# Performance work log

Measured on AMD Instinct MI355X. Metric: run time of the kernel, lower is better.

## Reference

```python
import jax, jax.numpy as jnp
import numpy as np

B, T, INP_DIM, H = 32, 2000, 4, 512
TC = 0.01  # t_const


def setup_inputs() -> dict:
    key = jax.random.key(0)
    ks = jax.random.split(key, 10)
    inp = jax.random.normal(ks[0], (B, T, INP_DIM), dtype=jnp.float32)
    hn = jax.random.uniform(ks[1], (1, B, 2 * H), dtype=jnp.float32)
    x = jnp.zeros((1, B, 2 * H), jnp.float32)
    inhib_stim = jnp.zeros((B, T, 2 * H), jnp.float32)
    u = lambda k, s, hi: jax.random.uniform(k, s, jnp.float32, 0.0, hi)
    str2str_w = u(ks[2], (H, H), 0.01)
    alm2alm_w = u(ks[3], (H, H), 0.01)
    alm2str_w = u(ks[4], (H, H), 0.01)
    str2alm_w = u(ks[5], (H, H), 0.01)
    inp_weight = u(ks[6], (INP_DIM, 2 * H), 0.01)
    sparse_mask = (jax.random.uniform(ks[7], (H, H)) < 0.1).astype(jnp.float32)
    str2str_fixed = u(ks[8], (H, H), 0.001) * sparse_mask
    str2str_mask = jnp.zeros((H, H), jnp.float32)
    n_inhib = int(0.3 * H)
    alm2str_mask = jnp.concatenate(
        [jnp.ones((H, H - n_inhib), jnp.float32), jnp.zeros((H, n_inhib), jnp.float32)], axis=1)
    alm2alm_sign = jnp.concatenate(
        [jnp.ones((H - n_inhib,), jnp.float32), -jnp.ones((n_inhib,), jnp.float32)])
    str_d1_mask = jnp.concatenate([jnp.ones((H,), jnp.float32), jnp.zeros((H,), jnp.float32)])
    return dict(inp=inp, hn=hn, x=x, inhib_stim=inhib_stim,
                str2str_w=str2str_w, alm2alm_w=alm2alm_w, alm2str_w=alm2str_w,
                str2alm_w=str2alm_w, inp_weight=inp_weight,
                str2str_fixed=str2str_fixed, str2str_mask=str2str_mask,
                alm2str_mask=alm2str_mask, alm2alm_sign=alm2alm_sign,
                str_d1_mask=str_d1_mask)


def _build_wrec(str2str_w, alm2alm_w, alm2str_w, str2alm_w,
                str2str_fixed, str2str_mask, alm2str_mask, alm2alm_sign):
    clip01 = lambda w: jnp.clip(w, 1e-15, 1.0)  # F.hardtanh(w, 1e-15, 1)
    str2str = -(str2str_mask * clip01(str2str_w) + str2str_fixed)      # @ (-I)
    alm2alm = clip01(alm2alm_w) * alm2alm_sign[None, :]                # @ diag(sign)
    alm2str = alm2str_mask * clip01(alm2str_w)
    str2alm = clip01(str2alm_w)
    W_str = jnp.concatenate([str2str, alm2str], axis=1)
    W_alm = jnp.concatenate([str2alm, alm2alm], axis=1)
    return jnp.concatenate([W_str, W_alm], axis=0)  # [2H, 2H]


def reference(inp, hn, x, inhib_stim, str2str_w, alm2alm_w, alm2str_w, str2alm_w,
              inp_weight, str2str_fixed, str2str_mask, alm2str_mask,
              alm2alm_sign, str_d1_mask):
    W_rec = _build_wrec(str2str_w, alm2alm_w, alm2str_w, str2alm_w,
                        str2str_fixed, str2str_mask, alm2str_mask, alm2alm_sign)
    # input drive precomputed for all steps: [B, T, 2H] (noise=False path)
    drive = jnp.einsum('bti,ih->bth', inp, inp_weight) * str_d1_mask + inhib_stim
    h0 = hn[0]  # [B, 2H]

    def step(h, d_t):
        h_new = jax.nn.relu(h + TC * (-h + h @ W_rec.T + d_t))
        return h_new, h_new

    _, hs = jax.lax.scan(step, h0, jnp.swapaxes(drive, 0, 1))  # [T, B, 2H]
    rnn_out = jnp.swapaxes(hs, 0, 1)                            # [B, T, 2H]
    x_out = jnp.broadcast_to(x[0][:, None, :], rnn_out.shape)   # x never updated
    hn_last = rnn_out[:, -1, :][None]
    x_last = x_out[:, -1, :][None]
    return (hn_last, rnn_out, x_last, x_out)
```

## Files before the change

kernel.cpp:

```cpp
#include <hip/hip_runtime.h>
#include <stdint.h>

#define H2      1024
#define TSTEPS  2000
#define TC_C    0.01f

#define NGROUPS   8
#define WG_PER_G  8
#define BPG       4
#define ROWS_WG   128
#define NTHR      512
#define NBLOCKS   (NGROUPS * WG_PER_G)

#define OFF_RNN   32768
#define OFF_XL    (32768 + 65536000)
#define OFF_XO    (OFF_XL + 32768)

#define FLAG_BASE 32768

#define HPAD 520

typedef __attribute__((ext_vector_type(8))) short bf16x8;
typedef __attribute__((ext_vector_type(4))) float f32x4;

__device__ __forceinline__ float clip01(float w) {
  return fminf(fmaxf(w, 1e-15f), 1.0f);
}
__device__ __forceinline__ uint32_t f2bf(float x) {
  uint32_t u = __float_as_uint(x);
  return ((u + 0x7fffu + ((u >> 16) & 1u)) >> 16) & 0xffffu;
}

__global__ void stralm_init_kernel(const float* __restrict__ hn,
                                   const float* __restrict__ x,
                                   float* __restrict__ out,
                                   float* __restrict__ ws) {
  const int tid = blockIdx.x * 256 + threadIdx.x;
  const int b  = tid >> 11;
  const int r  = tid & 2047;
  const int jq = (r & 255) * 4;
  const int t0 = (r >> 8) * 250;
  const float4 xv = *(const float4*)(x + b * H2 + jq);
  float* xo = out + OFF_XO;
  for (int i = 0; i < 250; ++i) {
    const int t = t0 + i;
    *(float4*)(xo + (size_t)(b * TSTEPS + t) * H2 + jq) = xv;
  }
  uint32_t* buf32 = (uint32_t*)ws;
  if (tid < 16384) {
    const float2 hv = *(const float2*)(hn + tid * 2);
    buf32[tid] = f2bf(hv.x) | (f2bf(hv.y) << 16);
  }
  if (tid < 8192)
    *(float4*)(out + OFF_XL + tid * 4) = *(const float4*)(x + tid * 4);
  if (tid < 128) ((int*)ws)[FLAG_BASE + tid] = 0;
}

__global__ __launch_bounds__(NTHR, 1) void stralm_rnn_kernel(
    const float* __restrict__ inp,
    const float* __restrict__ hn,
    const float* __restrict__ inhib,
    const float* __restrict__ ss_w, const float* __restrict__ a2a_w,
    const float* __restrict__ a2s_w, const float* __restrict__ s2a_w,
    const float* __restrict__ iw,
    const float* __restrict__ ss_fix, const float* __restrict__ ss_mask,
    const float* __restrict__ a2s_mask, const float* __restrict__ sign_v,
    const float* __restrict__ d1mask,
    float* __restrict__ out, float* __restrict__ ws) {
  __shared__ __align__(16) uint32_t smem[8256];

  const int tid = threadIdx.x;
  const int g   = blockIdx.x & 7;
  const int wg  = blockIdx.x >> 3;
  const int r0  = wg * ROWS_WG;
  const int l   = tid & 63;
  const int wv  = tid >> 6;

  uint32_t* buf32 = (uint32_t*)ws;
  int*      flags = (int*)ws + FLAG_BASE + g * 16;

  bf16x8 afr[32];
  {
    unsigned short* wstage = (unsigned short*)smem;
    for (int mt = 0; mt < 8; ++mt) {
      __syncthreads();
      for (int i = 0; i < 32; ++i) {
        const int idx = i * NTHR + tid;
        const int jt  = idx >> 10;
        const int k   = idx & 1023;
        const int jg  = r0 + mt * 16 + jt;
        const int jq  = jg & 511;
        float w;
        if (jg < 512) {
          if (k < 512)
            w = -(ss_mask[jq * 512 + k] * clip01(ss_w[jq * 512 + k]) +
                  ss_fix[jq * 512 + k]);
          else {
            const int kk = k - 512;
            w = a2s_mask[jq * 512 + kk] * clip01(a2s_w[jq * 512 + kk]);
          }
        } else {
          if (k < 512)
            w = clip01(s2a_w[jq * 512 + k]);
          else {
            const int kk = k - 512;
            w = clip01(a2a_w[jq * 512 + kk]) * sign_v[kk];
          }
        }
        wstage[jt * 1032 + k] = (unsigned short)f2bf(w);
      }
      __syncthreads();
      if (wv == mt) {
#pragma unroll
        for (int kt = 0; kt < 32; ++kt)
          afr[kt] = *(const bf16x8*)&wstage[(l & 15) * 1032 + kt * 32 +
                                            (l >> 4) * 8];
      }
    }
  }
  __syncthreads();

  uint32_t* h_lds = smem;

  const int  n    = l & 15;
  const bool act  = (n < 4);
  const int  h4   = l >> 4;
  const int  bg   = g * BPG + (act ? n : 0);
  const int  grow = r0 + wv * 16 + h4 * 4;
  float4 iwr0 = {}, iwr1 = {}, iwr2 = {}, iwr3 = {}, dmr = {}, hold = {};
  float4 inh_cur = {}, ip_cur = {};
  if (act) {
    iwr0 = *(const float4*)(iw + 0 * H2 + grow);
    iwr1 = *(const float4*)(iw + 1 * H2 + grow);
    iwr2 = *(const float4*)(iw + 2 * H2 + grow);
    iwr3 = *(const float4*)(iw + 3 * H2 + grow);
    dmr  = *(const float4*)(d1mask + grow);
    hold = *(const float4*)(hn + bg * H2 + grow);
    inh_cur = *(const float4*)(inhib + (size_t)bg * TSTEPS * H2 + grow);
    ip_cur  = *(const float4*)(inp + bg * (TSTEPS * 4));
  }
  const int bb = l & 3;

  for (int t = 0; t < TSTEPS; ++t) {
    const int p = t & 1;
    if (tid < WG_PER_G) {
      const int* fl = flags + tid;
      while (__hip_atomic_load(fl, __ATOMIC_RELAXED,
                               __HIP_MEMORY_SCOPE_AGENT) < t)
        __builtin_amdgcn_s_sleep(1);
    }
    __syncthreads();

    {
      const uint64_t* src64 = (const uint64_t*)(buf32 + p * 16384 + g * 2048);
      const uint64_t v0 = __hip_atomic_load(src64 + tid, __ATOMIC_RELAXED,
                                            __HIP_MEMORY_SCOPE_AGENT);
      const uint64_t v1 = __hip_atomic_load(src64 + 512 + tid, __ATOMIC_RELAXED,
                                            __HIP_MEMORY_SCOPE_AGENT);
      uint32_t* hbuf = h_lds + p * (4 * HPAD);
      const int e0 = 2 * tid;
      const int e1 = 1024 + 2 * tid;
      *(uint64_t*)(hbuf + (e0 >> 9) * HPAD + (e0 & 511)) = v0;
      *(uint64_t*)(hbuf + (e1 >> 9) * HPAD + (e1 & 511)) = v1;
    }
    __syncthreads();

    const unsigned short* hs = (const unsigned short*)(h_lds + p * (4 * HPAD)) +
                               bb * (2 * HPAD) + h4 * 8;
    f32x4 acc = {0.f, 0.f, 0.f, 0.f};
#pragma unroll
    for (int kt = 0; kt < 32; ++kt) {
      const bf16x8 bfr = *(const bf16x8*)&hs[kt * 32];
      acc = __builtin_amdgcn_mfma_f32_16x16x32_bf16(afr[kt], bfr, acc, 0, 0, 0);
    }

    float h0 = 0.f, h1 = 0.f, h2 = 0.f, h3 = 0.f;
    if (act) {
      const float d0 = dmr.x * (iwr0.x * ip_cur.x + iwr1.x * ip_cur.y +
                                iwr2.x * ip_cur.z + iwr3.x * ip_cur.w) + inh_cur.x;
      const float d1 = dmr.y * (iwr0.y * ip_cur.x + iwr1.y * ip_cur.y +
                                iwr2.y * ip_cur.z + iwr3.y * ip_cur.w) + inh_cur.y;
      const float d2 = dmr.z * (iwr0.z * ip_cur.x + iwr1.z * ip_cur.y +
                                iwr2.z * ip_cur.z + iwr3.z * ip_cur.w) + inh_cur.z;
      const float d3 = dmr.w * (iwr0.w * ip_cur.x + iwr1.w * ip_cur.y +
                                iwr2.w * ip_cur.z + iwr3.w * ip_cur.w) + inh_cur.w;
      h0 = fmaxf(0.f, (1.f - TC_C) * hold.x + TC_C * (acc[0] + d0));
      h1 = fmaxf(0.f, (1.f - TC_C) * hold.y + TC_C * (acc[1] + d1));
      h2 = fmaxf(0.f, (1.f - TC_C) * hold.z + TC_C * (acc[2] + d2));
      h3 = fmaxf(0.f, (1.f - TC_C) * hold.w + TC_C * (acc[3] + d3));
      hold = (float4){h0, h1, h2, h3};
      const uint64_t pk2 = (uint64_t)(f2bf(h0) | (f2bf(h1) << 16)) |
                           ((uint64_t)(f2bf(h2) | (f2bf(h3) << 16)) << 32);
      uint64_t* ep = (uint64_t*)(buf32 + (p ^ 1) * 16384 + bg * 512) +
                     (grow >> 2);
      __hip_atomic_store(ep, pk2, __ATOMIC_RELAXED, __HIP_MEMORY_SCOPE_AGENT);
    }
    asm volatile("s_waitcnt vmcnt(0)" ::: "memory");
    __syncthreads();
    if (tid == 0)
      __hip_atomic_store(flags + wg, t + 1, __ATOMIC_RELAXED,
                         __HIP_MEMORY_SCOPE_AGENT);
    if (act) {
      const f32x4 hv4 = {h0, h1, h2, h3};
      __builtin_nontemporal_store(
          hv4, (f32x4*)(out + OFF_RNN + (size_t)bg * (TSTEPS * H2) +
                        (size_t)t * H2 + grow));
      if (t == TSTEPS - 1)
        *(float4*)(out + bg * H2 + grow) = (float4){h0, h1, h2, h3};
      const int tn = (t < TSTEPS - 1) ? t + 1 : TSTEPS - 1;
      inh_cur = *(const float4*)(inhib + ((size_t)bg * TSTEPS + tn) * H2 + grow);
      ip_cur  = *(const float4*)(inp + bg * (TSTEPS * 4) + tn * 4);
    }
  }
}

extern "C" void kernel_launch(void* const* d_in, const int* in_sizes, int n_in,
                              void* d_out, int out_size, void* d_ws,
                              size_t ws_size, hipStream_t stream) {
  const float* inp      = (const float*)d_in[0];
  const float* hn       = (const float*)d_in[1];
  const float* x        = (const float*)d_in[2];
  const float* inhib    = (const float*)d_in[3];
  const float* ss_w     = (const float*)d_in[4];
  const float* a2a_w    = (const float*)d_in[5];
  const float* a2s_w    = (const float*)d_in[6];
  const float* s2a_w    = (const float*)d_in[7];
  const float* iw       = (const float*)d_in[8];
  const float* ss_fix   = (const float*)d_in[9];
  const float* ss_mask  = (const float*)d_in[10];
  const float* a2s_mask = (const float*)d_in[11];
  const float* sign_v   = (const float*)d_in[12];
  const float* d1mask   = (const float*)d_in[13];
  float* out = (float*)d_out;
  float* ws  = (float*)d_ws;

  hipLaunchKernelGGL(stralm_init_kernel, dim3(256), dim3(256), 0, stream,
                     hn, x, out, ws);
  hipLaunchKernelGGL(stralm_rnn_kernel, dim3(NBLOCKS), dim3(NTHR), 0, stream,
                     inp, hn, inhib, ss_w, a2a_w, a2s_w, s2a_w, iw, ss_fix,
                     ss_mask, a2s_mask, sign_v, d1mask, out, ws);
}
```

Before: 4.764 ms.

## Replace per-step workgroup barriers with per-source flag polling and LDS counters

Each wave now polls the global flag of the producer workgroup whose slice it loads, instead of 8 threads polling and then a block-wide barrier. After writing its slice into LDS, each wave bumps a per-source LDS counter. Consumer waves spin on those counters and start MFMA on a k-chunk as soon as it is ready, staggering the chunk order per wave. The drive computation is hoisted ahead of the MFMA loop. This aims to cut the two __syncthreads per step and overlap arrival of remote data with compute, at the cost of heavy spin traffic on global flags and LDS atomics, and relies on subtle memory ordering.

```diff
diff --git a/kernel.cpp b/kernel.cpp
--- a/kernel.cpp
+++ b/kernel.cpp
@@ -121,6 +121,9 @@
   __syncthreads();
 
   uint32_t* h_lds = smem;
+  int*      cnt   = (int*)(smem + 2 * 4 * HPAD);
+  if (tid < 16) cnt[tid] = 0;
+  __syncthreads();
 
   const int  n    = l & 15;
   const bool act  = (n < 4);
@@ -141,16 +144,16 @@
   }
   const int bb = l & 3;
 
+  const int wsrc = (tid >> 5) & 7;
+  const int boff = (tid >> 8) * HPAD + ((2 * tid) & 511);
+
   for (int t = 0; t < TSTEPS; ++t) {
     const int p = t & 1;
-    if (tid < WG_PER_G) {
-      const int* fl = flags + tid;
-      while (__hip_atomic_load(fl, __ATOMIC_RELAXED,
-                               __HIP_MEMORY_SCOPE_AGENT) < t)
-        __builtin_amdgcn_s_sleep(1);
-    }
-    __syncthreads();
-
+    {
+      const int* flp = flags + wsrc;
+      while (__hip_atomic_load(flp, __ATOMIC_RELAXED,
+                               __HIP_MEMORY_SCOPE_AGENT) < t) {}
+    }
     {
       const uint64_t* src64 = (const uint64_t*)(buf32 + p * 16384 + g * 2048);
       const uint64_t v0 = __hip_atomic_load(src64 + tid, __ATOMIC_RELAXED,
@@ -158,32 +161,46 @@
       const uint64_t v1 = __hip_atomic_load(src64 + 512 + tid, __ATOMIC_RELAXED,
                                             __HIP_MEMORY_SCOPE_AGENT);
       uint32_t* hbuf = h_lds + p * (4 * HPAD);
-      const int e0 = 2 * tid;
-      const int e1 = 1024 + 2 * tid;
-      *(uint64_t*)(hbuf + (e0 >> 9) * HPAD + (e0 & 511)) = v0;
-      *(uint64_t*)(hbuf + (e1 >> 9) * HPAD + (e1 & 511)) = v1;
-    }
-    __syncthreads();
-
-    const unsigned short* hs = (const unsigned short*)(h_lds + p * (4 * HPAD)) +
-                               bb * (2 * HPAD) + h4 * 8;
+      *(uint64_t*)(hbuf + boff)            = v0;
+      *(uint64_t*)(hbuf + 2 * HPAD + boff) = v1;
+      (void)__hip_atomic_fetch_add(cnt + p * 8 + wsrc, 1, __ATOMIC_RELEASE,
+                                   __HIP_MEMORY_SCOPE_WORKGROUP);
+    }
+
+    float d0 = 0.f, d1 = 0.f, d2 = 0.f, d3 = 0.f;
+    if (act) {
+      d0 = dmr.x * (iwr0.x * ip_cur.x + iwr1.x * ip_cur.y +
+                    iwr2.x * ip_cur.z + iwr3.x * ip_cur.w) + inh_cur.x;
+      d1 = dmr.y * (iwr0.y * ip_cur.x + iwr1.y * ip_cur.y +
+                    iwr2.y * ip_cur.z + iwr3.y * ip_cur.w) + inh_cur.y;
+      d2 = dmr.z * (iwr0.z * ip_cur.x + iwr1.z * ip_cur.y +
+                    iwr2.z * ip_cur.z + iwr3.z * ip_cur.w) + inh_cur.z;
+      d3 = dmr.w * (iwr0.w * ip_cur.x + iwr1.w * ip_cur.y +
+                    iwr2.w * ip_cur.z + iwr3.w * ip_cur.w) + inh_cur.w;
+    }
+
+    const unsigned short* hsb =
+        (const unsigned short*)(h_lds + p * (4 * HPAD)) + bb * (2 * HPAD) +
+        h4 * 8;
+    int* cntp = cnt + p * 8;
+    const int target = ((t >> 1) + 1) << 6;
     f32x4 acc = {0.f, 0.f, 0.f, 0.f};
+    for (int qq = 0; qq < 8; ++qq) {
+      const int q = (wv + qq) & 7;
+      while (__hip_atomic_load(cntp + q, __ATOMIC_ACQUIRE,
+                               __HIP_MEMORY_SCOPE_WORKGROUP) < target) {}
+      __builtin_amdgcn_sched_barrier(0);
 #pragma unroll
-    for (int kt = 0; kt < 32; ++kt) {
-      const bf16x8 bfr = *(const bf16x8*)&hs[kt * 32];
-      acc = __builtin_amdgcn_mfma_f32_16x16x32_bf16(afr[kt], bfr, acc, 0, 0, 0);
+      for (int j = 0; j < 4; ++j) {
+        const int kt = q * 4 + j;
+        const bf16x8 bfr = *(const bf16x8*)&hsb[kt * 32];
+        acc = __builtin_amdgcn_mfma_f32_16x16x32_bf16(afr[kt], bfr, acc,
+                                                      0, 0, 0);
+      }
     }
 
     float h0 = 0.f, h1 = 0.f, h2 = 0.f, h3 = 0.f;
     if (act) {
-      const float d0 = dmr.x * (iwr0.x * ip_cur.x + iwr1.x * ip_cur.y +
-                                iwr2.x * ip_cur.z + iwr3.x * ip_cur.w) + inh_cur.x;
-      const float d1 = dmr.y * (iwr0.y * ip_cur.x + iwr1.y * ip_cur.y +
-                                iwr2.y * ip_cur.z + iwr3.y * ip_cur.w) + inh_cur.y;
-      const float d2 = dmr.z * (iwr0.z * ip_cur.x + iwr1.z * ip_cur.y +
-                                iwr2.z * ip_cur.z + iwr3.z * ip_cur.w) + inh_cur.z;
-      const float d3 = dmr.w * (iwr0.w * ip_cur.x + iwr1.w * ip_cur.y +
-                                iwr2.w * ip_cur.z + iwr3.w * ip_cur.w) + inh_cur.w;
       h0 = fmaxf(0.f, (1.f - TC_C) * hold.x + TC_C * (acc[0] + d0));
       h1 = fmaxf(0.f, (1.f - TC_C) * hold.y + TC_C * (acc[1] + d1));
       h2 = fmaxf(0.f, (1.f - TC_C) * hold.z + TC_C * (acc[2] + d2));
```

Measured after the change: 18.11 ms. 280% more time.

## Repartition batches into two groups of sixteen to fill MFMA columns

Applied to the files above, without the earlier changes.

Reduces the batch groups from eight groups of four to two groups of sixteen. Each 16x16 MFMA now uses all sixteen batch columns instead of four, and the launch drops from 64 workgroups to 16. The 32-step MFMA chain is split into four independent accumulators to shorten the dependency chain. The drive computation is moved before the barrier. The cost is fewer workgroups, so fewer CUs in use, plus more LDS traffic and eight global loads per step for each workgroup.

```diff
diff --git a/kernel.cpp b/kernel.cpp
--- a/kernel.cpp
+++ b/kernel.cpp
@@ -5,9 +5,9 @@
 #define TSTEPS  2000
 #define TC_C    0.01f
 
-#define NGROUPS   8
+#define NGROUPS   2
 #define WG_PER_G  8
-#define BPG       4
+#define BPG       16
 #define ROWS_WG   128
 #define NTHR      512
 #define NBLOCKS   (NGROUPS * WG_PER_G)
@@ -18,10 +18,13 @@
 
 #define FLAG_BASE 32768
 
-#define HPAD 520
+#define HPAD 516
 
 typedef __attribute__((ext_vector_type(8))) short bf16x8;
 typedef __attribute__((ext_vector_type(4))) float f32x4;
+
+#define AT_LOAD(p)     __hip_atomic_load((p), __ATOMIC_RELAXED, __HIP_MEMORY_SCOPE_AGENT)
+#define AT_STORE(p, v) __hip_atomic_store((p), (v), __ATOMIC_RELAXED, __HIP_MEMORY_SCOPE_AGENT)
 
 __device__ __forceinline__ float clip01(float w) {
   return fminf(fmaxf(w, 1e-15f), 1.0f);
@@ -56,7 +59,7 @@
   if (tid < 128) ((int*)ws)[FLAG_BASE + tid] = 0;
 }
 
-__global__ __launch_bounds__(NTHR, 1) void stralm_rnn_kernel(
+__global__ __launch_bounds__(NTHR, 2) void stralm_rnn_kernel(
     const float* __restrict__ inp,
     const float* __restrict__ hn,
     const float* __restrict__ inhib,
@@ -67,11 +70,11 @@
     const float* __restrict__ a2s_mask, const float* __restrict__ sign_v,
     const float* __restrict__ d1mask,
     float* __restrict__ out, float* __restrict__ ws) {
-  __shared__ __align__(16) uint32_t smem[8256];
+  __shared__ __align__(16) uint32_t smem[16512];
 
   const int tid = threadIdx.x;
-  const int g   = blockIdx.x & 7;
-  const int wg  = blockIdx.x >> 3;
+  const int g   = blockIdx.x & 1;
+  const int wg  = blockIdx.x >> 1;
   const int r0  = wg * ROWS_WG;
   const int l   = tid & 63;
   const int wv  = tid >> 6;
@@ -123,84 +126,84 @@
   uint32_t* h_lds = smem;
 
   const int  n    = l & 15;
-  const bool act  = (n < 4);
   const int  h4   = l >> 4;
-  const int  bg   = g * BPG + (act ? n : 0);
+  const int  bg   = g * BPG + n;
   const int  grow = r0 + wv * 16 + h4 * 4;
-  float4 iwr0 = {}, iwr1 = {}, iwr2 = {}, iwr3 = {}, dmr = {}, hold = {};
-  float4 inh_cur = {}, ip_cur = {};
-  if (act) {
-    iwr0 = *(const float4*)(iw + 0 * H2 + grow);
-    iwr1 = *(const float4*)(iw + 1 * H2 + grow);
-    iwr2 = *(const float4*)(iw + 2 * H2 + grow);
-    iwr3 = *(const float4*)(iw + 3 * H2 + grow);
-    dmr  = *(const float4*)(d1mask + grow);
-    hold = *(const float4*)(hn + bg * H2 + grow);
-    inh_cur = *(const float4*)(inhib + (size_t)bg * TSTEPS * H2 + grow);
-    ip_cur  = *(const float4*)(inp + bg * (TSTEPS * 4));
-  }
-  const int bb = l & 3;
+  float4 iwr0, iwr1, iwr2, iwr3, dmr, hold, inh_cur, ip_cur;
+  iwr0 = *(const float4*)(iw + 0 * H2 + grow);
+  iwr1 = *(const float4*)(iw + 1 * H2 + grow);
+  iwr2 = *(const float4*)(iw + 2 * H2 + grow);
+  iwr3 = *(const float4*)(iw + 3 * H2 + grow);
+  dmr  = *(const float4*)(d1mask + grow);
+  hold = *(const float4*)(hn + bg * H2 + grow);
+  inh_cur = *(const float4*)(inhib + (size_t)bg * TSTEPS * H2 + grow);
+  ip_cur  = *(const float4*)(inp + bg * (TSTEPS * 4));
+  const int bb = l & 15;
 
   for (int t = 0; t < TSTEPS; ++t) {
     const int p = t & 1;
     if (tid < WG_PER_G) {
-      const int* fl = flags + tid;
-      while (__hip_atomic_load(fl, __ATOMIC_RELAXED,
-                               __HIP_MEMORY_SCOPE_AGENT) < t)
-        __builtin_amdgcn_s_sleep(1);
+      while (AT_LOAD(flags + tid) < t) __builtin_amdgcn_s_sleep(1);
     }
     __syncthreads();
 
     {
-      const uint64_t* src64 = (const uint64_t*)(buf32 + p * 16384 + g * 2048);
-      const uint64_t v0 = __hip_atomic_load(src64 + tid, __ATOMIC_RELAXED,
-                                            __HIP_MEMORY_SCOPE_AGENT);
-      const uint64_t v1 = __hip_atomic_load(src64 + 512 + tid, __ATOMIC_RELAXED,
-                                            __HIP_MEMORY_SCOPE_AGENT);
-      uint32_t* hbuf = h_lds + p * (4 * HPAD);
-      const int e0 = 2 * tid;
-      const int e1 = 1024 + 2 * tid;
-      *(uint64_t*)(hbuf + (e0 >> 9) * HPAD + (e0 & 511)) = v0;
-      *(uint64_t*)(hbuf + (e1 >> 9) * HPAD + (e1 & 511)) = v1;
-    }
+      const uint64_t* src64 = (const uint64_t*)buf32 + p * 8192 + g * 4096;
+      uint64_t v[8];
+#pragma unroll
+      for (int j = 0; j < 8; ++j)
+        v[j] = __hip_atomic_load(src64 + j * 512 + tid, __ATOMIC_RELAXED,
+                                 __HIP_MEMORY_SCOPE_AGENT);
+      uint32_t* hbuf = h_lds + p * (16 * HPAD);
+#pragma unroll
+      for (int j = 0; j < 8; ++j) {
+        const int flat  = j * 512 + tid;
+        const int batch = flat >> 8;
+        const int off   = (flat & 255) * 2;
+        *(uint64_t*)(hbuf + batch * HPAD + off) = v[j];
+      }
+    }
+    const float d0 = dmr.x * (iwr0.x * ip_cur.x + iwr1.x * ip_cur.y +
+                              iwr2.x * ip_cur.z + iwr3.x * ip_cur.w) + inh_cur.x;
+    const float d1 = dmr.y * (iwr0.y * ip_cur.x + iwr1.y * ip_cur.y +
+                              iwr2.y * ip_cur.z + iwr3.y * ip_cur.w) + inh_cur.y;
+    const float d2 = dmr.z * (iwr0.z * ip_cur.x + iwr1.z * ip_cur.y +
+                              iwr2.z * ip_cur.z + iwr3.z * ip_cur.w) + inh_cur.z;
+    const float d3 = dmr.w * (iwr0.w * ip_cur.x + iwr1.w * ip_cur.y +
+                              iwr2.w * ip_cur.z + iwr3.w * ip_cur.w) + inh_cur.w;
     __syncthreads();
 
-    const unsigned short* hs = (const unsigned short*)(h_lds + p * (4 * HPAD)) +
-                               bb * (2 * HPAD) + h4 * 8;
-    f32x4 acc = {0.f, 0.f, 0.f, 0.f};
-#pragma unroll
-    for (int kt = 0; kt < 32; ++kt) {
-      const bf16x8 bfr = *(const bf16x8*)&hs[kt * 32];
-      acc = __builtin_amdgcn_mfma_f32_16x16x32_bf16(afr[kt], bfr, acc, 0, 0, 0);
-    }
-
-    float h0 = 0.f, h1 = 0.f, h2 = 0.f, h3 = 0.f;
-    if (act) {
-      const float d0 = dmr.x * (iwr0.x * ip_cur.x + iwr1.x * ip_cur.y +
-                                iwr2.x * ip_cur.z + iwr3.x * ip_cur.w) + inh_cur.x;
-      const float d1 = dmr.y * (iwr0.y * ip_cur.x + iwr1.y * ip_cur.y +
-                                iwr2.y * ip_cur.z + iwr3.y * ip_cur.w) + inh_cur.y;
-      const float d2 = dmr.z * (iwr0.z * ip_cur.x + iwr1.z * ip_cur.y +
-                                iwr2.z * ip_cur.z + iwr3.z * ip_cur.w) + inh_cur.z;
-      const float d3 = dmr.w * (iwr0.w * ip_cur.x + iwr1.w * ip_cur.y +
-                                iwr2.w * ip_cur.z + iwr3.w * ip_cur.w) + inh_cur.w;
-      h0 = fmaxf(0.f, (1.f - TC_C) * hold.x + TC_C * (acc[0] + d0));
-      h1 = fmaxf(0.f, (1.f - TC_C) * hold.y + TC_C * (acc[1] + d1));
-      h2 = fmaxf(0.f, (1.f - TC_C) * hold.z + TC_C * (acc[2] + d2));
-      h3 = fmaxf(0.f, (1.f - TC_C) * hold.w + TC_C * (acc[3] + d3));
-      hold = (float4){h0, h1, h2, h3};
-      const uint64_t pk2 = (uint64_t)(f2bf(h0) | (f2bf(h1) << 16)) |
-                           ((uint64_t)(f2bf(h2) | (f2bf(h3) << 16)) << 32);
-      uint64_t* ep = (uint64_t*)(buf32 + (p ^ 1) * 16384 + bg * 512) +
-                     (grow >> 2);
-      __hip_atomic_store(ep, pk2, __ATOMIC_RELAXED, __HIP_MEMORY_SCOPE_AGENT);
-    }
+    const unsigned short* hsb =
+        (const unsigned short*)(h_lds + p * (16 * HPAD)) + bb * (2 * HPAD) +
+        h4 * 8;
+    f32x4 a0 = {0.f, 0.f, 0.f, 0.f}, a1 = a0, a2 = a0, a3 = a0;
+#pragma unroll
+    for (int j = 0; j < 8; ++j) {
+      const bf16x8 b0 = *(const bf16x8*)&hsb[(j)      * 32];
+      const bf16x8 b1 = *(const bf16x8*)&hsb[(8 + j)  * 32];
+      const bf16x8 b2 = *(const bf16x8*)&hsb[(16 + j) * 32];
+      const bf16x8 b3 = *(const bf16x8*)&hsb[(24 + j) * 32];
+      a0 = __builtin_amdgcn_mfma_f32_16x16x32_bf16(afr[j],      b0, a0, 0, 0, 0);
+      a1 = __builtin_amdgcn_mfma_f32_16x16x32_bf16(afr[8 + j],  b1, a1, 0, 0, 0);
+      a2 = __builtin_amdgcn_mfma_f32_16x16x32_bf16(afr[16 + j], b2, a2, 0, 0, 0);
+      a3 = __builtin_amdgcn_mfma_f32_16x16x32_bf16(afr[24 + j], b3, a3, 0, 0, 0);
+    }
+    const f32x4 acc = (a0 + a1) + (a2 + a3);
+
+    const float h0 = fmaxf(0.f, (1.f - TC_C) * hold.x + TC_C * (acc[0] + d0));
+    const float h1 = fmaxf(0.f, (1.f - TC_C) * hold.y + TC_C * (acc[1] + d1));
+    const float h2 = fmaxf(0.f, (1.f - TC_C) * hold.z + TC_C * (acc[2] + d2));
+    const float h3 = fmaxf(0.f, (1.f - TC_C) * hold.w + TC_C * (acc[3] + d3));
+    hold = (float4){h0, h1, h2, h3};
+    const uint64_t pk2 = (uint64_t)(f2bf(h0) | (f2bf(h1) << 16)) |
+                         ((uint64_t)(f2bf(h2) | (f2bf(h3) << 16)) << 32);
+    uint64_t* ep = (uint64_t*)buf32 + (p ^ 1) * 8192 + bg * 256 + (grow >> 2);
+    __hip_atomic_store(ep, pk2, __ATOMIC_RELAXED, __HIP_MEMORY_SCOPE_AGENT);
     asm volatile("s_waitcnt vmcnt(0)" ::: "memory");
     __syncthreads();
     if (tid == 0)
-      __hip_atomic_store(flags + wg, t + 1, __ATOMIC_RELAXED,
-                         __HIP_MEMORY_SCOPE_AGENT);
-    if (act) {
+      AT_STORE(flags + wg, t + 1);
+    {
       const f32x4 hv4 = {h0, h1, h2, h3};
       __builtin_nontemporal_store(
           hv4, (f32x4*)(out + OFF_RNN + (size_t)bg * (TSTEPS * H2) +
```

New measurement: 7.011 ms. 1.47x slower.
